# Kernel optimization log

Hardware: AMD Instinct MI355X
Metric: run time of the kernel (lower is better)

Reference implementation:

```python
import jax, jax.numpy as jnp
import numpy as np

B, H, W = 1, 48, 160
CIN, CF, D = 1024, 64, 48  # input_features, PSM_features, depth_channel = max_disp/downsample
EPS = 1e-5


def setup_inputs() -> dict:
    key = jax.random.key(0)
    ks = jax.random.split(key, 12)
    z = lambda s: jnp.zeros(s, jnp.float32)
    o = lambda s: jnp.ones(s, jnp.float32)
    return {
        "left_features": jax.random.normal(ks[0], (B, CIN, H, W), jnp.float32),
        "right_features": jax.random.normal(ks[1], (B, CIN, H, W), jnp.float32),
        "conv1_w": jax.random.normal(ks[2], (CF, CIN), jnp.float32) * 0.03,
        "conv1_b": z((CF,)),
        "bn1_g": o((CF,)), "bn1_b": z((CF,)),
        "bn1_m": jax.random.normal(ks[3], (CF,), jnp.float32) * 0.1,
        "bn1_v": jax.random.uniform(ks[4], (CF,), jnp.float32) + 0.5,
        "c3a_w": jax.random.normal(ks[5], (CF, 2 * CF, 3, 3, 3), jnp.float32) * 0.02,
        "c3a_b": z((CF,)),
        "bn3a_g": o((CF,)), "bn3a_b": z((CF,)),
        "bn3a_m": jax.random.normal(ks[6], (CF,), jnp.float32) * 0.1,
        "bn3a_v": jax.random.uniform(ks[7], (CF,), jnp.float32) + 0.5,
        "c3b_w": jax.random.normal(ks[8], (CF, CF, 3, 3, 3), jnp.float32) * 0.02,
        "c3b_b": z((CF,)),
        "bn3b_g": o((CF,)), "bn3b_b": z((CF,)),
        "bn3b_m": jax.random.normal(ks[9], (CF,), jnp.float32) * 0.1,
        "bn3b_v": jax.random.uniform(ks[10], (CF,), jnp.float32) + 0.5,
    }


def _bn(x, g, b, m, v, nsp):
    # eval-mode batchnorm; nsp = number of trailing spatial dims
    sh = (-1,) + (1,) * nsp
    return (x - m.reshape(sh)) * (g.reshape(sh) * jax.lax.rsqrt(v.reshape(sh) + EPS)) + b.reshape(sh)


def reference(left_features, right_features, conv1_w, conv1_b, bn1_g, bn1_b, bn1_m, bn1_v,
              c3a_w, c3a_b, bn3a_g, bn3a_b, bn3a_m, bn3a_v,
              c3b_w, c3b_b, bn3b_g, bn3b_b, bn3b_m, bn3b_v):
    def down(x):
        y = jnp.einsum('oi,bihw->bohw', conv1_w, x) + conv1_b[:, None, None]
        return jax.nn.relu(_bn(y, bn1_g, bn1_b, bn1_m, bn1_v, 2))

    L = down(left_features)   # [B,CF,H,W]
    R = down(right_features)  # [B,CF,H,W]

    # Vectorized shifted cost volume (replaces the Python loop over disparities).
    # For disparity d, output width j: left -> L[...,j] if j>=d else 0; right -> R[...,j-d] if j>=d else 0.
    idx = jnp.arange(W)[None, :] - jnp.arange(D)[:, None]       # [D,W]
    mask = (idx >= 0).astype(L.dtype)                           # [D,W]
    left_vol = L[:, :, :, None, :] * mask                       # [B,CF,H,D,W]
    right_vol = R[:, :, :, jnp.clip(idx, 0, W - 1)] * mask      # [B,CF,H,D,W]
    cost = jnp.concatenate([left_vol, right_vol], axis=1)       # [B,2CF,H,D,W]
    cost = jnp.transpose(cost, (0, 1, 3, 2, 4))                 # [B,2CF,D,H,W]

    def conv3(x, wk, bias):
        y = jax.lax.conv_general_dilated(x, wk, (1, 1, 1), [(1, 1)] * 3,
                                         dimension_numbers=('NCDHW', 'OIDHW', 'NCDHW'))
        return y + bias[:, None, None, None]

    y = jax.nn.relu(_bn(conv3(cost, c3a_w, c3a_b), bn3a_g, bn3a_b, bn3a_m, bn3a_v, 3))
    y = jax.nn.relu(_bn(conv3(y, c3b_w, c3b_b), bn3b_g, bn3b_b, bn3b_m, bn3b_v, 3))
    return y.reshape(B, -1, H, W)  # [B, CF*D, H, W]
```

## Files before the change

kernel.cpp:

```cpp
#include <hip/hip_runtime.h>
#include <hip/hip_bf16.h>


#define HH   48
#define WW   160
#define DDEP 48
#define CIN  1024
#define NPX  (HH*WW)

typedef unsigned short u16;
typedef unsigned int   u32;
typedef __attribute__((ext_vector_type(8))) short bf16x8;
typedef __attribute__((ext_vector_type(4))) float f32x4;
typedef __attribute__((ext_vector_type(4))) u32   u32x4;

__device__ __forceinline__ u16 f2bf(float f) {
    u32 u = __builtin_bit_cast(u32, f);
    u32 r = u + 0x7FFFu + ((u >> 16) & 1u);
    return (u16)(r >> 16);
}

__global__ __launch_bounds__(256) void k_prep(
    const float* __restrict__ c3a, const float* __restrict__ c3b,
    const float* __restrict__ cb3a, const float* __restrict__ g3a,
    const float* __restrict__ b3a,  const float* __restrict__ m3a,
    const float* __restrict__ v3a,
    const float* __restrict__ cb3b, const float* __restrict__ g3b,
    const float* __restrict__ b3b,  const float* __restrict__ m3b,
    const float* __restrict__ v3b,
    u16* __restrict__ wa, u16* __restrict__ wb, float* __restrict__ bnc)
{
    int tid = blockIdx.x*256 + threadIdx.x;
    if (tid < 221184) {
        int i = tid & 127, o = (tid >> 7) & 63, tap = tid >> 13;
        wa[tid] = f2bf(c3a[(o*128 + i)*27 + tap]);
    } else {
        int t2 = tid - 221184;
        if (t2 < 110592) {
            int i = t2 & 63;
            int kw = (t2 >> 6) % 3;
            int rest = t2 / 192;
            int o = rest & 63, kdkh = rest >> 6;
            wb[t2] = f2bf(c3b[(o*64 + i)*27 + (kdkh/3)*9 + (kdkh%3)*3 + kw]);
        }
    }
    if (tid < 64) {
        float s = g3a[tid] * rsqrtf(v3a[tid] + 1e-5f);
        bnc[tid]      = s;
        bnc[64 + tid] = (cb3a[tid] - m3a[tid])*s + b3a[tid];
    } else if (tid < 128) {
        int o = tid - 64;
        float s = g3b[o] * rsqrtf(v3b[o] + 1e-5f);
        bnc[128 + o] = s;
        bnc[192 + o] = (cb3b[o] - m3b[o])*s + b3b[o];
    }
}

__global__ __launch_bounds__(256) void k_conv1(
    const float* __restrict__ left, const float* __restrict__ right,
    const float* __restrict__ w1, const float* __restrict__ b1,
    const float* __restrict__ g,  const float* __restrict__ bb,
    const float* __restrict__ m,  const float* __restrict__ v,
    u16* __restrict__ outLR)
{
    const int img = blockIdx.y;
    const float* x = img ? right : left;
    u16* out = outLR + (size_t)img*NPX*64;
    const int px = blockIdx.x*64 + (threadIdx.x & 63);
    const int o0 = (threadIdx.x >> 6)*16;

    float acc[16];
    #pragma unroll
    for (int oo = 0; oo < 16; ++oo) acc[oo] = 0.f;

    for (int i = 0; i < CIN; i += 4) {
        float x0 = x[(i+0)*NPX + px];
        float x1 = x[(i+1)*NPX + px];
        float x2 = x[(i+2)*NPX + px];
        float x3 = x[(i+3)*NPX + px];
        #pragma unroll
        for (int oo = 0; oo < 16; ++oo) {
            const float4 wv4 = *(const float4*)(w1 + (size_t)(o0+oo)*CIN + i);
            acc[oo] = fmaf(wv4.w, x3, fmaf(wv4.z, x2,
                      fmaf(wv4.y, x1, fmaf(wv4.x, x0, acc[oo]))));
        }
    }
    u16 res[16];
    #pragma unroll
    for (int oo = 0; oo < 16; ++oo) {
        int o = o0 + oo;
        float s = g[o] * rsqrtf(v[o] + 1e-5f);
        float val = (acc[oo] + b1[o] - m[o])*s + bb[o];
        res[oo] = f2bf(val > 0.f ? val : 0.f);
    }
    u16* dst = out + (size_t)px*64 + o0;
    *(u32x4*)dst       = *(const u32x4*)res;
    *(u32x4*)(dst + 8) = *(const u32x4*)(res + 8);
}

__global__ __launch_bounds__(256) void k_conv3a(
    const u16* __restrict__ LRb, const u16* __restrict__ wa,
    const float* __restrict__ bnc, u16* __restrict__ yt)
{
    __shared__ u16 sm[31744];
    u16* Lt = sm;
    u16* Rt = sm + 11520;
    u16* Aw = sm + 23040;

    const int h  = blockIdx.x;
    const int d0 = blockIdx.y*2;
    const int tid = threadIdx.x;
    const int l  = tid & 63;
    const int wv = tid >> 6;
    const int dd = wv >> 1;
    const int wbase = (wv & 1)*80;
    const int l15 = l & 15, l4 = l >> 4;
    const int wcol = wbase + l15;
    const bf16x8 bzero = {0,0,0,0,0,0,0,0};

    f32x4 acc[4][5];
    #pragma unroll
    for (int a = 0; a < 4; ++a)
        #pragma unroll
        for (int b = 0; b < 5; ++b)
            acc[a][b] = (f32x4){0.f,0.f,0.f,0.f};

    for (int kh = 0; kh < 3; ++kh) {
        int hp = h + kh - 1;
        if (hp < 0 || hp >= HH) continue;
        __syncthreads();
        {
            const u16* ls = LRb + (size_t)hp*WW*64;
            const u16* rs = LRb + (size_t)NPX*64 + (size_t)hp*WW*64;
            #pragma unroll
            for (int gq = 0; gq < 5; ++gq) {
                int eb = (gq*256 + tid)*8;
                int wwi = eb >> 6, ii = eb & 63;
                u32x4 va = *(const u32x4*)(ls + eb);
                u32x4 vb = *(const u32x4*)(rs + eb);
                *(u32x4*)(Lt + wwi*72 + ii) = va;
                *(u32x4*)(Rt + wwi*72 + ii) = vb;
            }
        }
        for (int kd = 0; kd < 3; ++kd) {
            int dp = d0 + dd + kd - 1;
            bool dok = (dp >= 0) && (dp < DDEP);
            for (int kw = 0; kw < 3; ++kw) {
                __syncthreads();
                {
                    const u16* as = wa + (size_t)(kd*9 + kh*3 + kw)*8192;
                    #pragma unroll
                    for (int gq = 0; gq < 4; ++gq) {
                        int eb = (gq*256 + tid)*8;
                        int o = eb >> 7, ii = eb & 127;
                        *(u32x4*)(Aw + o*136 + ii) = *(const u32x4*)(as + eb);
                    }
                }
                __syncthreads();

                int laddr[5], raddr[5];
                bool val[5];
                #pragma unroll
                for (int nf = 0; nf < 5; ++nf) {
                    int wp = wcol + nf*16 + kw - 1;
                    bool vv = dok && (wp >= 0) && (wp < WW) && (wp >= dp);
                    val[nf]   = vv;
                    laddr[nf] = (vv ? wp : 0)*72;
                    raddr[nf] = (vv ? (wp - dp) : 0)*72;
                }
                #pragma unroll
                for (int ic = 0; ic < 4; ++ic) {
                    const int kcolA = ic*32 + 8*l4;
                    bf16x8 a0 = *(const bf16x8*)(Aw + ( 0 + l15)*136 + kcolA);
                    bf16x8 a1 = *(const bf16x8*)(Aw + (16 + l15)*136 + kcolA);
                    bf16x8 a2 = *(const bf16x8*)(Aw + (32 + l15)*136 + kcolA);
                    bf16x8 a3 = *(const bf16x8*)(Aw + (48 + l15)*136 + kcolA);
                    const int kin = (ic & 1)*32 + 8*l4;
                    #pragma unroll
                    for (int nf = 0; nf < 5; ++nf) {
                        const u16* bp = (ic < 2) ? (Lt + laddr[nf] + kin)
                                                 : (Rt + raddr[nf] + kin);
                        bf16x8 b = *(const bf16x8*)bp;
                        b = val[nf] ? b : bzero;
                        acc[0][nf] = __builtin_amdgcn_mfma_f32_16x16x32_bf16(a0, b, acc[0][nf], 0, 0, 0);
                        acc[1][nf] = __builtin_amdgcn_mfma_f32_16x16x32_bf16(a1, b, acc[1][nf], 0, 0, 0);
                        acc[2][nf] = __builtin_amdgcn_mfma_f32_16x16x32_bf16(a2, b, acc[2][nf], 0, 0, 0);
                        acc[3][nf] = __builtin_amdgcn_mfma_f32_16x16x32_bf16(a3, b, acc[3][nf], 0, 0, 0);
                    }
                }
            }
        }
    }

    __syncthreads();
    u16* eps = sm + wv*5280;
    float sc[4][4], sh[4][4];
    #pragma unroll
    for (int mf = 0; mf < 4; ++mf)
        #pragma unroll
        for (int r = 0; r < 4; ++r) {
            int o = mf*16 + 4*l4 + r;
            sc[mf][r] = bnc[o];
            sh[mf][r] = bnc[64 + o];
        }
    #pragma unroll
    for (int mf = 0; mf < 4; ++mf)
        #pragma unroll
        for (int nf = 0; nf < 5; ++nf)
            #pragma unroll
            for (int r = 0; r < 4; ++r) {
                float vv = acc[mf][nf][r]*sc[mf][r] + sh[mf][r];
                vv = vv > 0.f ? vv : 0.f;
                eps[(nf*16 + l15)*66 + mf*16 + 4*l4 + r] = f2bf(vv);
            }
    const size_t rowbase = (size_t)((d0 + dd)*HH + h)*WW + wbase;
    u16* yb = yt + rowbase*64;
    #pragma unroll
    for (int k = 0; k < 40; ++k) {
        int flat = k*64 + l;
        int n = flat >> 5, odw = (flat & 31)*2;
        u32 vv = *(const u32*)(eps + n*66 + odw);
        *(u32*)(yb + (size_t)n*64 + odw) = vv;
    }
}

__global__ __launch_bounds__(256) void k_conv3b(
    const u16* __restrict__ yt, const u16* __restrict__ wb,
    const float* __restrict__ bnc, float* __restrict__ outp)
{
    __shared__ u16 sm2[35840];
    u16* Bt0 = sm2;
    u16* Bt1 = sm2 + 11520;
    u16* A2  = sm2 + 23040;

    const int h  = blockIdx.x;
    const int d0 = blockIdx.y*2;
    const int tid = threadIdx.x;
    const int l  = tid & 63;
    const int wv = tid >> 6;
    const int dd = wv >> 1;
    const int wbase = (wv & 1)*80;
    const int l15 = l & 15, l4 = l >> 4;
    const int wcol = wbase + l15;
    const bf16x8 bzero = {0,0,0,0,0,0,0,0};

    f32x4 acc[4][5];
    #pragma unroll
    for (int a = 0; a < 4; ++a)
        #pragma unroll
        for (int b = 0; b < 5; ++b)
            acc[a][b] = (f32x4){0.f,0.f,0.f,0.f};

    for (int kh = 0; kh < 3; ++kh) {
        int hp = h + kh - 1;
        if (hp < 0 || hp >= HH) continue;
        for (int kd = 0; kd < 3; ++kd) {
            __syncthreads();
            {
                int dpa = d0 + kd - 1, dpb = d0 + kd;
                int ca = min(max(dpa, 0), DDEP-1);
                int cb = min(max(dpb, 0), DDEP-1);
                const u16* s0 = yt + ((size_t)(ca*HH + hp)*WW)*64;
                const u16* s1 = yt + ((size_t)(cb*HH + hp)*WW)*64;
                #pragma unroll
                for (int gq = 0; gq < 5; ++gq) {
                    int eb = (gq*256 + tid)*8;
                    int wwi = eb >> 6, ii = eb & 63;
                    *(u32x4*)(Bt0 + wwi*72 + ii) = *(const u32x4*)(s0 + eb);
                    *(u32x4*)(Bt1 + wwi*72 + ii) = *(const u32x4*)(s1 + eb);
                }
                const u16* as = wb + (size_t)(kd*3 + kh)*12288;
                #pragma unroll
                for (int gq = 0; gq < 6; ++gq) {
                    int idx = gq*256 + tid;
                    int o = idx/24;
                    int c = (idx - o*24)*8;
                    *(u32x4*)(A2 + o*200 + c) = *(const u32x4*)(as + (size_t)idx*8);
                }
            }
            __syncthreads();

            int dpw = d0 + dd + kd - 1;
            bool dok = (dpw >= 0) && (dpw < DDEP);
            const u16* Bt = dd ? Bt1 : Bt0;
            for (int kw = 0; kw < 3; ++kw) {
                int baddr[5]; bool val[5];
                #pragma unroll
                for (int nf = 0; nf < 5; ++nf) {
                    int wp = wcol + nf*16 + kw - 1;
                    bool vv = dok && (wp >= 0) && (wp < WW);
                    val[nf]   = vv;
                    baddr[nf] = (vv ? wp : 0)*72;
                }
                #pragma unroll
                for (int ic = 0; ic < 2; ++ic) {
                    const int kcolA = kw*64 + ic*32 + 8*l4;
                    bf16x8 a0 = *(const bf16x8*)(A2 + ( 0 + l15)*200 + kcolA);
                    bf16x8 a1 = *(const bf16x8*)(A2 + (16 + l15)*200 + kcolA);
                    bf16x8 a2 = *(const bf16x8*)(A2 + (32 + l15)*200 + kcolA);
                    bf16x8 a3 = *(const bf16x8*)(A2 + (48 + l15)*200 + kcolA);
                    const int kin = ic*32 + 8*l4;
                    #pragma unroll
                    for (int nf = 0; nf < 5; ++nf) {
                        bf16x8 b = *(const bf16x8*)(Bt + baddr[nf] + kin);
                        b = val[nf] ? b : bzero;
                        acc[0][nf] = __builtin_amdgcn_mfma_f32_16x16x32_bf16(a0, b, acc[0][nf], 0, 0, 0);
                        acc[1][nf] = __builtin_amdgcn_mfma_f32_16x16x32_bf16(a1, b, acc[1][nf], 0, 0, 0);
                        acc[2][nf] = __builtin_amdgcn_mfma_f32_16x16x32_bf16(a2, b, acc[2][nf], 0, 0, 0);
                        acc[3][nf] = __builtin_amdgcn_mfma_f32_16x16x32_bf16(a3, b, acc[3][nf], 0, 0, 0);
                    }
                }
            }
        }
    }

    const int dout = d0 + dd;
    #pragma unroll
    for (int mf = 0; mf < 4; ++mf)
        #pragma unroll
        for (int r = 0; r < 4; ++r) {
            int o = mf*16 + 4*l4 + r;
            float s = bnc[128 + o], t = bnc[192 + o];
            size_t base = ((size_t)(o*DDEP + dout)*HH + h)*WW + wbase;
            #pragma unroll
            for (int nf = 0; nf < 5; ++nf) {
                float vv = acc[mf][nf][r]*s + t;
                outp[base + nf*16 + l15] = vv > 0.f ? vv : 0.f;
            }
        }
}

extern "C" void kernel_launch(void* const* d_in, const int* in_sizes, int n_in,
                              void* d_out, int out_size, void* d_ws, size_t ws_size,
                              hipStream_t stream)
{
    const float* left  = (const float*)d_in[0];
    const float* right = (const float*)d_in[1];
    const float* w1    = (const float*)d_in[2];
    const float* b1    = (const float*)d_in[3];
    const float* g1    = (const float*)d_in[4];
    const float* bb1   = (const float*)d_in[5];
    const float* m1    = (const float*)d_in[6];
    const float* v1    = (const float*)d_in[7];
    const float* c3a   = (const float*)d_in[8];
    const float* cb3a  = (const float*)d_in[9];
    const float* g3a   = (const float*)d_in[10];
    const float* b3a   = (const float*)d_in[11];
    const float* m3a   = (const float*)d_in[12];
    const float* v3a   = (const float*)d_in[13];
    const float* c3b   = (const float*)d_in[14];
    const float* cb3b  = (const float*)d_in[15];
    const float* g3b   = (const float*)d_in[16];
    const float* b3b   = (const float*)d_in[17];
    const float* m3b   = (const float*)d_in[18];
    const float* v3b   = (const float*)d_in[19];

    char* ws = (char*)d_ws;
    u16*   LRb = (u16*)ws;
    u16*   wa  = (u16*)(ws + 1966080);
    u16*   wb  = (u16*)(ws + 1966080 + 442368);
    float* bnc = (float*)(ws + 1966080 + 442368 + 221184);
    u16*   yt  = (u16*)(ws + 1966080 + 442368 + 221184 + 1024);
    if (ws_size < 49816576) return;

    k_prep<<<dim3(1296), dim3(256), 0, stream>>>(
        c3a, c3b, cb3a, g3a, b3a, m3a, v3a, cb3b, g3b, b3b, m3b, v3b, wa, wb, bnc);
    k_conv1<<<dim3(120, 2), dim3(256), 0, stream>>>(
        left, right, w1, b1, g1, bb1, m1, v1, LRb);
    k_conv3a<<<dim3(48, 24), dim3(256), 0, stream>>>(LRb, wa, bnc, yt);
    k_conv3b<<<dim3(48, 24), dim3(256), 0, stream>>>(yt, wb, bnc, (float*)d_out);
}
```

Baseline: 384.9 us.

## Split conv1 reduction over input channels and add a separate reduce kernel

The 1x1 conv1 kernel is split along the 1024 input channels into 8 slices through a third grid dimension, so 1920 blocks run instead of 240 on a large GPU. Each slice writes fp32 partial sums to scratch space borrowed from the output buffer. A new reduce kernel sums the slices and applies bias, batchnorm, ReLU and bf16 conversion. This targets low occupancy and the long serial channel loop, at the cost of an extra kernel launch and about 31MB of partial-sum traffic.

```diff
diff --git a/kernel.cpp b/kernel.cpp
--- a/kernel.cpp
+++ b/kernel.cpp
@@ -7,12 +7,14 @@
 #define DDEP 48
 #define CIN  1024
 #define NPX  (HH*WW)
+#define KSPL 8
 
 typedef unsigned short u16;
 typedef unsigned int   u32;
 typedef __attribute__((ext_vector_type(8))) short bf16x8;
 typedef __attribute__((ext_vector_type(4))) float f32x4;
 typedef __attribute__((ext_vector_type(4))) u32   u32x4;
+typedef __attribute__((ext_vector_type(2))) u32   u32x2;
 
 __device__ __forceinline__ u16 f2bf(float f) {
     u32 u = __builtin_bit_cast(u32, f);
@@ -58,14 +60,11 @@
 
 __global__ __launch_bounds__(256) void k_conv1(
     const float* __restrict__ left, const float* __restrict__ right,
-    const float* __restrict__ w1, const float* __restrict__ b1,
-    const float* __restrict__ g,  const float* __restrict__ bb,
-    const float* __restrict__ m,  const float* __restrict__ v,
-    u16* __restrict__ outLR)
+    const float* __restrict__ w1, float* __restrict__ P)
 {
     const int img = blockIdx.y;
+    const int s   = blockIdx.z;
     const float* x = img ? right : left;
-    u16* out = outLR + (size_t)img*NPX*64;
     const int px = blockIdx.x*64 + (threadIdx.x & 63);
     const int o0 = (threadIdx.x >> 6)*16;
 
@@ -73,7 +72,9 @@
     #pragma unroll
     for (int oo = 0; oo < 16; ++oo) acc[oo] = 0.f;
 
-    for (int i = 0; i < CIN; i += 4) {
+    const int ibase = s*(CIN/KSPL);
+    for (int it = 0; it < CIN/KSPL; it += 4) {
+        const int i = ibase + it;
         float x0 = x[(i+0)*NPX + px];
         float x1 = x[(i+1)*NPX + px];
         float x2 = x[(i+2)*NPX + px];
@@ -85,17 +86,35 @@
                       fmaf(wv4.y, x1, fmaf(wv4.x, x0, acc[oo]))));
         }
     }
-    u16 res[16];
-    #pragma unroll
-    for (int oo = 0; oo < 16; ++oo) {
-        int o = o0 + oo;
-        float s = g[o] * rsqrtf(v[o] + 1e-5f);
-        float val = (acc[oo] + b1[o] - m[o])*s + bb[o];
-        res[oo] = f2bf(val > 0.f ? val : 0.f);
-    }
-    u16* dst = out + (size_t)px*64 + o0;
-    *(u32x4*)dst       = *(const u32x4*)res;
-    *(u32x4*)(dst + 8) = *(const u32x4*)(res + 8);
+    float* dst = P + ((size_t)(s*2 + img)*NPX + px)*64 + o0;
+    #pragma unroll
+    for (int q = 0; q < 4; ++q)
+        *(f32x4*)(dst + q*4) = *(const f32x4*)(acc + q*4);
+}
+
+__global__ __launch_bounds__(256) void k_conv1_reduce(
+    const float* __restrict__ P,
+    const float* __restrict__ b1,
+    const float* __restrict__ g,  const float* __restrict__ bb,
+    const float* __restrict__ m,  const float* __restrict__ v,
+    u16* __restrict__ LRb)
+{
+    const int tid = blockIdx.x*256 + threadIdx.x;
+    const int f = tid*4;
+    f32x4 acc = *(const f32x4*)(P + f);
+    #pragma unroll
+    for (int s = 1; s < KSPL; ++s)
+        acc += *(const f32x4*)(P + (size_t)(s*2)*(NPX*64) + f);
+    const int o0 = f & 63;
+    u16 res[4];
+    #pragma unroll
+    for (int r = 0; r < 4; ++r) {
+        int o = o0 + r;
+        float sc = g[o] * rsqrtf(v[o] + 1e-5f);
+        float val = (acc[r] + b1[o] - m[o])*sc + bb[o];
+        res[r] = f2bf(val > 0.f ? val : 0.f);
+    }
+    *(u32x2*)(LRb + f) = *(const u32x2*)res;
 }
 
 __global__ __launch_bounds__(256) void k_conv3a(
@@ -363,10 +382,14 @@
     u16*   yt  = (u16*)(ws + 1966080 + 442368 + 221184 + 1024);
     if (ws_size < 49816576) return;
 
+    float* P = (float*)d_out;
+
     k_prep<<<dim3(1296), dim3(256), 0, stream>>>(
         c3a, c3b, cb3a, g3a, b3a, m3a, v3a, cb3b, g3b, b3b, m3b, v3b, wa, wb, bnc);
-    k_conv1<<<dim3(120, 2), dim3(256), 0, stream>>>(
-        left, right, w1, b1, g1, bb1, m1, v1, LRb);
+    k_conv1<<<dim3(120, 2, KSPL), dim3(256), 0, stream>>>(
+        left, right, w1, P);
+    k_conv1_reduce<<<dim3(960), dim3(256), 0, stream>>>(
+        P, b1, g1, bb1, m1, v1, LRb);
     k_conv3a<<<dim3(48, 24), dim3(256), 0, stream>>>(LRb, wa, bnc, yt);
     k_conv3b<<<dim3(48, 24), dim3(256), 0, stream>>>(yt, wb, bnc, (float*)d_out);
 }
```

Result: no change. 384.4 us (-0.1%).
